# Performance work log

Measured on AMD Instinct MI355X. Metric: run time of the kernel, lower is better.

Reference implementation:

```python
import jax, jax.numpy as jnp
import numpy as np

DISCOUNT_FACTOR = 0.99
EPS = 1e-8


def setup_inputs() -> dict:
    key = jax.random.key(0)
    k1, k2, k3 = jax.random.split(key, 3)
    B, S = 8192, 1024
    # raw params initialized exactly like the torch module: atanh(target)
    raw_gamma = jnp.arctanh(jnp.array([DISCOUNT_FACTOR], dtype=jnp.float32))
    # create_init_lambda_sequence(0.5, S): linear ramp with mean == AVERAGE_LAMBDA
    lam_init = jnp.linspace(0.1, 0.9, S).astype(jnp.float32)
    raw_lambd = jnp.arctanh(lam_init)
    values = jax.random.normal(k1, (B, S + 1, 1), dtype=jnp.float32)
    rewards = jax.random.normal(k2, (B, S, 1), dtype=jnp.float32)
    dones = jax.random.randint(k3, (B, S, 1), 0, 2).astype(jnp.int32)
    return {
        "raw_gamma": raw_gamma,
        "raw_lambd": raw_lambd,
        "values": values,
        "rewards": rewards,
        "dones": dones,
        "input_seq_len": 1024,
    }


def reference(raw_gamma, raw_lambd, values, rewards, dones, input_seq_len):
    # gamma / lambd properties: tanh then clamp_min(1e-8)
    gamma = jnp.maximum(jnp.tanh(raw_gamma), EPS)[0]            # scalar
    lambd = jnp.maximum(jnp.tanh(raw_lambd), EPS)               # [max_seq_len]
    lam_seq = lambd[-input_seq_len:]                            # [S]

    # ---- update_sum_reward_weights (runs under no_grad in torch) ----
    # backward recurrence: v[t] = gamma * (1 - lam[t] + lam[t] * v[t+1]),  v[S] = 1
    def w_step(v_next, lam_t):
        v_t = gamma * (1.0 - lam_t + lam_t * v_next)
        return v_t, jnp.maximum(1.0 - v_t, EPS)

    _, w = jax.lax.scan(
        w_step,
        jnp.asarray(1.0, values.dtype),
        jax.lax.stop_gradient(lam_seq),
        reverse=True,
    )  # w: [S]
    srw = w / jnp.maximum(w.mean(), EPS)
    sum_reward_weights = jax.lax.stop_gradient(srw)[None, :, None]  # [1, S, 1]

    # ---- calculate_lambda_returns ----
    # ret[t] = r[t] + gamma*(1-done[t]) * ((1-lam[t])*V[t+1] + lam[t]*ret[t+1])
    d = dones.astype(values.dtype)
    v_next = values[:, 1:, :]                                   # [B, S, 1]
    xs = (
        jnp.swapaxes(rewards, 0, 1),   # [S, B, 1]
        jnp.swapaxes(d, 0, 1),         # [S, B, 1]
        jnp.swapaxes(v_next, 0, 1),    # [S, B, 1]
        lam_seq,                       # [S]
    )

    def r_step(ret_next, x):
        r, dn, vn, lam = x
        ret = r + gamma * (1.0 - dn) * ((1.0 - lam) * vn + lam * ret_next)
        return ret, ret

    _, rets = jax.lax.scan(r_step, values[:, -1, :], xs, reverse=True)  # [S, B, 1]
    lambda_returns = jnp.swapaxes(rets, 0, 1)                           # [B, S, 1]
    return lambda_returns, sum_reward_weights
```

## Files before the change

kernel.cpp:

```cpp
#include <hip/hip_runtime.h>
#include <math.h>

#define EPSF 1e-8f

typedef float nvec4 __attribute__((ext_vector_type(4)));
typedef int   nivec4 __attribute__((ext_vector_type(4)));

__device__ __forceinline__ float pick(nvec4 v, int i) {
    return i == 0 ? v.x : i == 1 ? v.y : i == 2 ? v.z : v.w;
}

__device__ __forceinline__ void suffix_scan64(float& A, float& B, int lane) {
#pragma unroll
    for (int d = 1; d < 64; d <<= 1) {
        float Ao = __shfl_down(A, d);
        float Bo = __shfl_down(B, d);
        if (lane + d < 64) {
            A = fmaf(B, Ao, A);
            B = B * Bo;
        }
    }
}

__global__ __launch_bounds__(256, 8)
void td_kernel(const float* __restrict__ raw_gamma,
               const float* __restrict__ raw_lambd, int lam_off,
               const float* __restrict__ values,
               const float* __restrict__ rewards,
               const int* __restrict__ dones,
               float* __restrict__ out, int B, int S)
{
    __shared__ float sA[4], sB[4];
    const int lane = threadIdx.x & 63;
    const int c    = threadIdx.x >> 6;
    const float gamma = fmaxf(tanhf(raw_gamma[0]), EPSF);

    if ((int)blockIdx.x == B) {
        if (threadIdx.x >= 64) return;
        const int base = lane << 4;
        float a[16], b[16];
#pragma unroll
        for (int k = 0; k < 4; ++k) {
            float4 l4 = *(const float4*)(raw_lambd + lam_off + base + 4 * k);
            float lv[4] = {l4.x, l4.y, l4.z, l4.w};
#pragma unroll
            for (int j = 0; j < 4; ++j) {
                float g1 = gamma * fmaxf(tanhf(lv[j]), EPSF);
                b[4 * k + j] = g1;
                a[4 * k + j] = gamma - g1;
            }
        }
        float A = a[15], Bc = b[15];
#pragma unroll
        for (int j = 14; j >= 0; --j) { A = fmaf(b[j], A, a[j]); Bc *= b[j]; }
        suffix_scan64(A, Bc, lane);
        float EA = __shfl_down(A, 1);
        float EB = __shfl_down(Bc, 1);
        if (lane == 63) { EA = 0.0f; EB = 1.0f; }
        float v = EA + EB;
        float w[16], sum = 0.0f;
#pragma unroll
        for (int j = 15; j >= 0; --j) {
            v = fmaf(b[j], v, a[j]);
            w[j] = fmaxf(1.0f - v, EPSF);
            sum += w[j];
        }
#pragma unroll
        for (int d = 32; d; d >>= 1) sum += __shfl_xor(sum, d);
        float inv = 1.0f / fmaxf(sum / (float)S, EPSF);
        float* srw = out + (size_t)B * S;
#pragma unroll
        for (int j = 0; j < 16; ++j) srw[base + j] = w[j] * inv;
        return;
    }

    const int r  = blockIdx.x;
    const int C  = S >> 2;
    const int t0 = c * C + (lane << 2);
    const size_t rb = (size_t)r * (S + 1);

    nvec4  r4 = __builtin_nontemporal_load((const nvec4*)(rewards + (size_t)r * S + t0));
    nivec4 d4 = __builtin_nontemporal_load((const nivec4*)(dones + (size_t)r * S + t0));

    const int sh = (r + 1) & 3;
    const size_t E  = rb + (size_t)c * C + 1;
    const size_t A0 = E - sh;
    nvec4 m4 = __builtin_nontemporal_load((const nvec4*)(values + A0) + lane);
    size_t A0t = A0 + 256;
    const size_t last4 = (size_t)B * (S + 1) - 4;
    if (A0t > last4) A0t = last4;
    nvec4 t4 = __builtin_nontemporal_load((const nvec4*)(values + A0t));
    const int delta = (int)(A0 + 256 - A0t);
    float vS = values[rb + S];

    float4 l4 = *(const float4*)(raw_lambd + lam_off + t0);
    float lv[4] = {l4.x, l4.y, l4.z, l4.w};
    float g1v[4];
#pragma unroll
    for (int j = 0; j < 4; ++j)
        g1v[j] = gamma * fmaxf(tanhf(lv[j]), EPSF);

    float n0 = __shfl_down(m4.x, 1);
    float n1 = __shfl_down(m4.y, 1);
    float n2 = __shfl_down(m4.z, 1);
    if (lane == 63) {
        n0 = pick(t4, delta);
        n1 = pick(t4, delta + 1 > 3 ? 3 : delta + 1);
        n2 = pick(t4, delta + 2 > 3 ? 3 : delta + 2);
    }
    float vn0, vn1, vn2, vn3;
    if (sh == 0)      { vn0 = m4.x; vn1 = m4.y; vn2 = m4.z; vn3 = m4.w; }
    else if (sh == 1) { vn0 = m4.y; vn1 = m4.z; vn2 = m4.w; vn3 = n0; }
    else if (sh == 2) { vn0 = m4.z; vn1 = m4.w; vn2 = n0;   vn3 = n1; }
    else              { vn0 = m4.w; vn1 = n0;   vn2 = n1;   vn3 = n2; }

    float vn[4] = {vn0, vn1, vn2, vn3};
    float rr[4] = {r4.x, r4.y, r4.z, r4.w};
    int   di[4] = {d4.x, d4.y, d4.z, d4.w};
    float a[4], b[4];
#pragma unroll
    for (int j = 0; j < 4; ++j) {
        float ndn = 1.0f - (float)di[j];
        b[j] = g1v[j] * ndn;
        a[j] = fmaf((gamma - g1v[j]) * vn[j], ndn, rr[j]);
    }

    float A = a[3], Bc = b[3];
#pragma unroll
    for (int j = 2; j >= 0; --j) { A = fmaf(b[j], A, a[j]); Bc *= b[j]; }
    suffix_scan64(A, Bc, lane);
    float EA = __shfl_down(A, 1);
    float EB = __shfl_down(Bc, 1);
    if (lane == 63) { EA = 0.0f; EB = 1.0f; }
    if (lane == 0) { sA[c] = A; sB[c] = Bc; }
    __syncthreads();

    float x = vS;
#pragma unroll
    for (int j = 3; j >= 1; --j)
        if (j > c) x = fmaf(sB[j], x, sA[j]);

    float xi = fmaf(EB, x, EA);
    float o3 = fmaf(b[3], xi, a[3]);
    float o2 = fmaf(b[2], o3, a[2]);
    float o1 = fmaf(b[1], o2, a[1]);
    float o0 = fmaf(b[0], o1, a[0]);
    nvec4 ov = {o0, o1, o2, o3};
    __builtin_nontemporal_store(ov, (nvec4*)(out + (size_t)r * S + t0));
}

extern "C" void kernel_launch(void* const* d_in, const int* in_sizes, int n_in,
                              void* d_out, int out_size, void* d_ws, size_t ws_size,
                              hipStream_t stream) {
    const float* raw_gamma = (const float*)d_in[0];
    const float* raw_lambd = (const float*)d_in[1];
    const float* values    = (const float*)d_in[2];
    const float* rewards   = (const float*)d_in[3];
    const int*   dones     = (const int*)d_in[4];
    float* out = (float*)d_out;

    int n_v = in_sizes[2];
    int n_r = in_sizes[3];
    int B = n_v - n_r;
    int S = n_r / B;
    int lam_off = in_sizes[1] - S;

    td_kernel<<<B + 1, 256, 0, stream>>>(
        raw_gamma, raw_lambd, lam_off, values, rewards, dones, out, B, S);
}
```

Before: 139.0 us.

## Map one wavefront per row with 16 elements per lane, dropping block sync

New measurement: 161.5 us. +16.1%, slower.

```diff
diff --git a/kernel.cpp b/kernel.cpp
--- a/kernel.cpp
+++ b/kernel.cpp
@@ -22,7 +22,7 @@
     }
 }
 
-__global__ __launch_bounds__(256, 8)
+__global__ __launch_bounds__(256, 4)
 void td_kernel(const float* __restrict__ raw_gamma,
                const float* __restrict__ raw_lambd, int lam_off,
                const float* __restrict__ values,
@@ -30,12 +30,12 @@
                const int* __restrict__ dones,
                float* __restrict__ out, int B, int S)
 {
-    __shared__ float sA[4], sB[4];
     const int lane = threadIdx.x & 63;
-    const int c    = threadIdx.x >> 6;
+    const int w    = threadIdx.x >> 6;
     const float gamma = fmaxf(tanhf(raw_gamma[0]), EPSF);
-
-    if ((int)blockIdx.x == B) {
+    const int nb = (B + 3) >> 2;
+
+    if ((int)blockIdx.x == nb) {
         if (threadIdx.x >= 64) return;
         const int base = lane << 4;
         float a[16], b[16];
@@ -58,95 +58,127 @@
         float EB = __shfl_down(Bc, 1);
         if (lane == 63) { EA = 0.0f; EB = 1.0f; }
         float v = EA + EB;
-        float w[16], sum = 0.0f;
+        float wv[16], sum = 0.0f;
 #pragma unroll
         for (int j = 15; j >= 0; --j) {
             v = fmaf(b[j], v, a[j]);
-            w[j] = fmaxf(1.0f - v, EPSF);
-            sum += w[j];
+            wv[j] = fmaxf(1.0f - v, EPSF);
+            sum += wv[j];
         }
 #pragma unroll
         for (int d = 32; d; d >>= 1) sum += __shfl_xor(sum, d);
         float inv = 1.0f / fmaxf(sum / (float)S, EPSF);
         float* srw = out + (size_t)B * S;
 #pragma unroll
-        for (int j = 0; j < 16; ++j) srw[base + j] = w[j] * inv;
+        for (int j = 0; j < 16; ++j) srw[base + j] = wv[j] * inv;
         return;
     }
 
-    const int r  = blockIdx.x;
-    const int C  = S >> 2;
-    const int t0 = c * C + (lane << 2);
+    const int r = ((int)blockIdx.x << 2) + w;
+    if (r >= B) return;
+    const int t0 = lane << 4;
     const size_t rb = (size_t)r * (S + 1);
 
-    nvec4  r4 = __builtin_nontemporal_load((const nvec4*)(rewards + (size_t)r * S + t0));
-    nivec4 d4 = __builtin_nontemporal_load((const nivec4*)(dones + (size_t)r * S + t0));
+    nvec4 r4[4]; nivec4 d4[4];
+    const nvec4*  rp = (const nvec4*)(rewards + (size_t)r * S + t0);
+    const nivec4* dp = (const nivec4*)(dones + (size_t)r * S + t0);
+#pragma unroll
+    for (int k = 0; k < 4; ++k) {
+        r4[k] = __builtin_nontemporal_load(rp + k);
+        d4[k] = __builtin_nontemporal_load(dp + k);
+    }
 
     const int sh = (r + 1) & 3;
-    const size_t E  = rb + (size_t)c * C + 1;
+    const size_t E  = rb + t0 + 1;
     const size_t A0 = E - sh;
-    nvec4 m4 = __builtin_nontemporal_load((const nvec4*)(values + A0) + lane);
-    size_t A0t = A0 + 256;
+    nvec4 m[4];
+#pragma unroll
+    for (int k = 0; k < 4; ++k)
+        m[k] = __builtin_nontemporal_load((const nvec4*)(values + A0) + k);
+    size_t A0t = A0 + 16;
     const size_t last4 = (size_t)B * (S + 1) - 4;
     if (A0t > last4) A0t = last4;
     nvec4 t4 = __builtin_nontemporal_load((const nvec4*)(values + A0t));
-    const int delta = (int)(A0 + 256 - A0t);
+    const int delta = (int)(A0 + 16 - A0t);
     float vS = values[rb + S];
 
-    float4 l4 = *(const float4*)(raw_lambd + lam_off + t0);
-    float lv[4] = {l4.x, l4.y, l4.z, l4.w};
-    float g1v[4];
-#pragma unroll
-    for (int j = 0; j < 4; ++j)
-        g1v[j] = gamma * fmaxf(tanhf(lv[j]), EPSF);
-
-    float n0 = __shfl_down(m4.x, 1);
-    float n1 = __shfl_down(m4.y, 1);
-    float n2 = __shfl_down(m4.z, 1);
+    float g1v[16];
+#pragma unroll
+    for (int k = 0; k < 4; ++k) {
+        float4 l4 = *(const float4*)(raw_lambd + lam_off + t0 + 4 * k);
+        g1v[4 * k + 0] = gamma * fmaxf(tanhf(l4.x), EPSF);
+        g1v[4 * k + 1] = gamma * fmaxf(tanhf(l4.y), EPSF);
+        g1v[4 * k + 2] = gamma * fmaxf(tanhf(l4.z), EPSF);
+        g1v[4 * k + 3] = gamma * fmaxf(tanhf(l4.w), EPSF);
+    }
+
+    float cov[16] = {m[0].x, m[0].y, m[0].z, m[0].w,
+                     m[1].x, m[1].y, m[1].z, m[1].w,
+                     m[2].x, m[2].y, m[2].z, m[2].w,
+                     m[3].x, m[3].y, m[3].z, m[3].w};
+    float n0 = __shfl_down(m[0].x, 1);
+    float n1 = __shfl_down(m[0].y, 1);
+    float n2 = __shfl_down(m[0].z, 1);
     if (lane == 63) {
         n0 = pick(t4, delta);
         n1 = pick(t4, delta + 1 > 3 ? 3 : delta + 1);
         n2 = pick(t4, delta + 2 > 3 ? 3 : delta + 2);
     }
-    float vn0, vn1, vn2, vn3;
-    if (sh == 0)      { vn0 = m4.x; vn1 = m4.y; vn2 = m4.z; vn3 = m4.w; }
-    else if (sh == 1) { vn0 = m4.y; vn1 = m4.z; vn2 = m4.w; vn3 = n0; }
-    else if (sh == 2) { vn0 = m4.z; vn1 = m4.w; vn2 = n0;   vn3 = n1; }
-    else              { vn0 = m4.w; vn1 = n0;   vn2 = n1;   vn3 = n2; }
-
-    float vn[4] = {vn0, vn1, vn2, vn3};
-    float rr[4] = {r4.x, r4.y, r4.z, r4.w};
-    int   di[4] = {d4.x, d4.y, d4.z, d4.w};
-    float a[4], b[4];
-#pragma unroll
-    for (int j = 0; j < 4; ++j) {
+    float vn[16];
+    if (sh == 0) {
+#pragma unroll
+        for (int i = 0; i < 16; ++i) vn[i] = cov[i];
+    } else if (sh == 1) {
+#pragma unroll
+        for (int i = 0; i < 15; ++i) vn[i] = cov[i + 1];
+        vn[15] = n0;
+    } else if (sh == 2) {
+#pragma unroll
+        for (int i = 0; i < 14; ++i) vn[i] = cov[i + 2];
+        vn[14] = n0; vn[15] = n1;
+    } else {
+#pragma unroll
+        for (int i = 0; i < 13; ++i) vn[i] = cov[i + 3];
+        vn[13] = n0; vn[14] = n1; vn[15] = n2;
+    }
+
+    float rr[16]; int di[16];
+#pragma unroll
+    for (int k = 0; k < 4; ++k) {
+        rr[4 * k + 0] = r4[k].x; rr[4 * k + 1] = r4[k].y;
+        rr[4 * k + 2] = r4[k].z; rr[4 * k + 3] = r4[k].w;
+        di[4 * k + 0] = d4[k].x; di[4 * k + 1] = d4[k].y;
+        di[4 * k + 2] = d4[k].z; di[4 * k + 3] = d4[k].w;
+    }
+
+    float a[16], b[16];
+#pragma unroll
+    for (int j = 0; j < 16; ++j) {
         float ndn = 1.0f - (float)di[j];
         b[j] = g1v[j] * ndn;
         a[j] = fmaf((gamma - g1v[j]) * vn[j], ndn, rr[j]);
     }
 
-    float A = a[3], Bc = b[3];
-#pragma unroll
-    for (int j = 2; j >= 0; --j) { A = fmaf(b[j], A, a[j]); Bc *= b[j]; }
+    float A = a[15], Bc = b[15];
+#pragma unroll
+    for (int j = 14; j >= 0; --j) { A = fmaf(b[j], A, a[j]); Bc *= b[j]; }
     suffix_scan64(A, Bc, lane);
     float EA = __shfl_down(A, 1);
     float EB = __shfl_down(Bc, 1);
     if (lane == 63) { EA = 0.0f; EB = 1.0f; }
-    if (lane == 0) { sA[c] = A; sB[c] = Bc; }
-    __syncthreads();
-
-    float x = vS;
-#pragma unroll
-    for (int j = 3; j >= 1; --j)
-        if (j > c) x = fmaf(sB[j], x, sA[j]);
-
-    float xi = fmaf(EB, x, EA);
-    float o3 = fmaf(b[3], xi, a[3]);
-    float o2 = fmaf(b[2], o3, a[2]);
-    float o1 = fmaf(b[1], o2, a[1]);
-    float o0 = fmaf(b[0], o1, a[0]);
-    nvec4 ov = {o0, o1, o2, o3};
-    __builtin_nontemporal_store(ov, (nvec4*)(out + (size_t)r * S + t0));
+
+    float x = fmaf(EB, vS, EA);
+    float o[16];
+    o[15] = fmaf(b[15], x, a[15]);
+#pragma unroll
+    for (int j = 14; j >= 0; --j) o[j] = fmaf(b[j], o[j + 1], a[j]);
+
+    nvec4* op = (nvec4*)(out + (size_t)r * S + t0);
+#pragma unroll
+    for (int k = 0; k < 4; ++k) {
+        nvec4 ov = {o[4 * k], o[4 * k + 1], o[4 * k + 2], o[4 * k + 3]};
+        __builtin_nontemporal_store(ov, op + k);
+    }
 }
 
 extern "C" void kernel_launch(void* const* d_in, const int* in_sizes, int n_in,
@@ -165,6 +197,7 @@
     int S = n_r / B;
     int lam_off = in_sizes[1] - S;
 
-    td_kernel<<<B + 1, 256, 0, stream>>>(
+    int nb = (B + 3) >> 2;
+    td_kernel<<<nb + 1, 256, 0, stream>>>(
         raw_gamma, raw_lambd, lam_off, values, rewards, dones, out, B, S);
 }
```

## Process four rows per block with double-buffered prefetch of next row

Applied to the files above, without the earlier changes.

Result: no change. 141.5 us (+1.7%).

```diff
diff --git a/kernel.cpp b/kernel.cpp
--- a/kernel.cpp
+++ b/kernel.cpp
@@ -22,7 +22,7 @@
     }
 }
 
-__global__ __launch_bounds__(256, 8)
+__global__ __launch_bounds__(256, 4)
 void td_kernel(const float* __restrict__ raw_gamma,
                const float* __restrict__ raw_lambd, int lam_off,
                const float* __restrict__ values,
@@ -30,13 +30,14 @@
                const int* __restrict__ dones,
                float* __restrict__ out, int B, int S)
 {
-    __shared__ float sA[4], sB[4];
+    __shared__ float sA[2][4], sB[2][4];
     const int lane = threadIdx.x & 63;
     const int c    = threadIdx.x >> 6;
-    const float gamma = fmaxf(tanhf(raw_gamma[0]), EPSF);
+    const int nb   = B >> 2;
 
-    if ((int)blockIdx.x == B) {
+    if ((int)blockIdx.x == nb) {
         if (threadIdx.x >= 64) return;
+        const float gamma = fmaxf(tanhf(raw_gamma[0]), EPSF);
         const int base = lane << 4;
         float a[16], b[16];
 #pragma unroll
@@ -74,79 +75,101 @@
         return;
     }
 
-    const int r  = blockIdx.x;
+    const float gamma = fmaxf(tanhf(raw_gamma[0]), EPSF);
     const int C  = S >> 2;
     const int t0 = c * C + (lane << 2);
-    const size_t rb = (size_t)r * (S + 1);
-
-    nvec4  r4 = __builtin_nontemporal_load((const nvec4*)(rewards + (size_t)r * S + t0));
-    nivec4 d4 = __builtin_nontemporal_load((const nivec4*)(dones + (size_t)r * S + t0));
-
-    const int sh = (r + 1) & 3;
-    const size_t E  = rb + (size_t)c * C + 1;
-    const size_t A0 = E - sh;
-    nvec4 m4 = __builtin_nontemporal_load((const nvec4*)(values + A0) + lane);
-    size_t A0t = A0 + 256;
-    const size_t last4 = (size_t)B * (S + 1) - 4;
-    if (A0t > last4) A0t = last4;
-    nvec4 t4 = __builtin_nontemporal_load((const nvec4*)(values + A0t));
-    const int delta = (int)(A0 + 256 - A0t);
-    float vS = values[rb + S];
 
     float4 l4 = *(const float4*)(raw_lambd + lam_off + t0);
     float lv[4] = {l4.x, l4.y, l4.z, l4.w};
-    float g1v[4];
-#pragma unroll
-    for (int j = 0; j < 4; ++j)
-        g1v[j] = gamma * fmaxf(tanhf(lv[j]), EPSF);
-
-    float n0 = __shfl_down(m4.x, 1);
-    float n1 = __shfl_down(m4.y, 1);
-    float n2 = __shfl_down(m4.z, 1);
-    if (lane == 63) {
-        n0 = pick(t4, delta);
-        n1 = pick(t4, delta + 1 > 3 ? 3 : delta + 1);
-        n2 = pick(t4, delta + 2 > 3 ? 3 : delta + 2);
-    }
-    float vn0, vn1, vn2, vn3;
-    if (sh == 0)      { vn0 = m4.x; vn1 = m4.y; vn2 = m4.z; vn3 = m4.w; }
-    else if (sh == 1) { vn0 = m4.y; vn1 = m4.z; vn2 = m4.w; vn3 = n0; }
-    else if (sh == 2) { vn0 = m4.z; vn1 = m4.w; vn2 = n0;   vn3 = n1; }
-    else              { vn0 = m4.w; vn1 = n0;   vn2 = n1;   vn3 = n2; }
-
-    float vn[4] = {vn0, vn1, vn2, vn3};
-    float rr[4] = {r4.x, r4.y, r4.z, r4.w};
-    int   di[4] = {d4.x, d4.y, d4.z, d4.w};
-    float a[4], b[4];
+    float g1v[4], av[4];
 #pragma unroll
     for (int j = 0; j < 4; ++j) {
-        float ndn = 1.0f - (float)di[j];
-        b[j] = g1v[j] * ndn;
-        a[j] = fmaf((gamma - g1v[j]) * vn[j], ndn, rr[j]);
+        g1v[j] = gamma * fmaxf(tanhf(lv[j]), EPSF);
+        av[j]  = gamma - g1v[j];
     }
 
-    float A = a[3], Bc = b[3];
+    const int r0 = (int)blockIdx.x << 2;
+    const size_t last4 = (size_t)B * (S + 1) - 4;
+
+    nvec4  r4[2]; nivec4 d4[2]; nvec4 m4[2], t4[2];
+    float  vS[2]; int dlt[2];
+
+#define ISSUE(BUF, RR) do {                                                     \
+        const int _r = (RR);                                                    \
+        r4[BUF] = __builtin_nontemporal_load(                                   \
+            (const nvec4*)(rewards + (size_t)_r * S + t0));                     \
+        d4[BUF] = __builtin_nontemporal_load(                                   \
+            (const nivec4*)(dones + (size_t)_r * S + t0));                      \
+        const size_t _rb = (size_t)_r * (S + 1);                                \
+        const int _sh = (_r + 1) & 3;                                           \
+        const size_t _A0 = _rb + (size_t)c * C + 1 - _sh;                       \
+        m4[BUF] = __builtin_nontemporal_load((const nvec4*)(values + _A0) + lane); \
+        size_t _A0t = _A0 + 256;                                                \
+        if (_A0t > last4) _A0t = last4;                                         \
+        t4[BUF] = __builtin_nontemporal_load((const nvec4*)(values + _A0t));    \
+        dlt[BUF] = (int)(_A0 + 256 - _A0t);                                     \
+        vS[BUF] = values[_rb + S];                                              \
+    } while (0)
+
+    ISSUE(0, r0);
+
 #pragma unroll
-    for (int j = 2; j >= 0; --j) { A = fmaf(b[j], A, a[j]); Bc *= b[j]; }
-    suffix_scan64(A, Bc, lane);
-    float EA = __shfl_down(A, 1);
-    float EB = __shfl_down(Bc, 1);
-    if (lane == 63) { EA = 0.0f; EB = 1.0f; }
-    if (lane == 0) { sA[c] = A; sB[c] = Bc; }
-    __syncthreads();
+    for (int i = 0; i < 4; ++i) {
+        const int cur = i & 1;
+        const int r   = r0 + i;
+        if (i < 3) ISSUE(cur ^ 1, r + 1);
 
-    float x = vS;
+        const int sh = (r + 1) & 3;
+        float n0 = __shfl_down(m4[cur].x, 1);
+        float n1 = __shfl_down(m4[cur].y, 1);
+        float n2 = __shfl_down(m4[cur].z, 1);
+        if (lane == 63) {
+            const int dd = dlt[cur];
+            n0 = pick(t4[cur], dd);
+            n1 = pick(t4[cur], dd + 1 > 3 ? 3 : dd + 1);
+            n2 = pick(t4[cur], dd + 2 > 3 ? 3 : dd + 2);
+        }
+        float vn0, vn1, vn2, vn3;
+        if (sh == 0)      { vn0 = m4[cur].x; vn1 = m4[cur].y; vn2 = m4[cur].z; vn3 = m4[cur].w; }
+        else if (sh == 1) { vn0 = m4[cur].y; vn1 = m4[cur].z; vn2 = m4[cur].w; vn3 = n0; }
+        else if (sh == 2) { vn0 = m4[cur].z; vn1 = m4[cur].w; vn2 = n0;        vn3 = n1; }
+        else              { vn0 = m4[cur].w; vn1 = n0;        vn2 = n1;        vn3 = n2; }
+
+        float vn[4] = {vn0, vn1, vn2, vn3};
+        float rr[4] = {r4[cur].x, r4[cur].y, r4[cur].z, r4[cur].w};
+        int   di[4] = {d4[cur].x, d4[cur].y, d4[cur].z, d4[cur].w};
+        float a[4], b[4];
 #pragma unroll
-    for (int j = 3; j >= 1; --j)
-        if (j > c) x = fmaf(sB[j], x, sA[j]);
+        for (int j = 0; j < 4; ++j) {
+            float ndn = 1.0f - (float)di[j];
+            b[j] = g1v[j] * ndn;
+            a[j] = fmaf(av[j] * vn[j], ndn, rr[j]);
+        }
 
-    float xi = fmaf(EB, x, EA);
-    float o3 = fmaf(b[3], xi, a[3]);
-    float o2 = fmaf(b[2], o3, a[2]);
-    float o1 = fmaf(b[1], o2, a[1]);
-    float o0 = fmaf(b[0], o1, a[0]);
-    nvec4 ov = {o0, o1, o2, o3};
-    __builtin_nontemporal_store(ov, (nvec4*)(out + (size_t)r * S + t0));
+        float A = a[3], Bc = b[3];
+#pragma unroll
+        for (int j = 2; j >= 0; --j) { A = fmaf(b[j], A, a[j]); Bc *= b[j]; }
+        suffix_scan64(A, Bc, lane);
+        float EA = __shfl_down(A, 1);
+        float EB = __shfl_down(Bc, 1);
+        if (lane == 63) { EA = 0.0f; EB = 1.0f; }
+        if (lane == 0) { sA[cur][c] = A; sB[cur][c] = Bc; }
+        __syncthreads();
+
+        float x = vS[cur];
+#pragma unroll
+        for (int j = 3; j >= 1; --j)
+            if (j > c) x = fmaf(sB[cur][j], x, sA[cur][j]);
+
+        float xi = fmaf(EB, x, EA);
+        float o3 = fmaf(b[3], xi, a[3]);
+        float o2 = fmaf(b[2], o3, a[2]);
+        float o1 = fmaf(b[1], o2, a[1]);
+        float o0 = fmaf(b[0], o1, a[0]);
+        nvec4 ov = {o0, o1, o2, o3};
+        __builtin_nontemporal_store(ov, (nvec4*)(out + (size_t)r * S + t0));
+    }
+#undef ISSUE
 }
 
 extern "C" void kernel_launch(void* const* d_in, const int* in_sizes, int n_in,
@@ -165,6 +188,7 @@
     int S = n_r / B;
     int lam_off = in_sizes[1] - S;
 
-    td_kernel<<<B + 1, 256, 0, stream>>>(
+    int nb = B >> 2;
+    td_kernel<<<nb + 1, 256, 0, stream>>>(
         raw_gamma, raw_lambd, lam_off, values, rewards, dones, out, B, S);
 }
```
